# Kernel tuning notes

Measured on AMD Instinct MI355X. Metric: run time of the kernel, lower is better.

The kernel has to match this reference:

```python
import jax, jax.numpy as jnp
import numpy as np

A, M, Q, H, T = 4096, 64, 64, 64, 4
BOX_L = 20.0


def _pairwise_displacements(positions, box):
    # Minimal-image pairwise displacements. dr[i, j] = r_j - r_i (PBC-wrapped).
    diff = positions[None, :, :] - positions[:, None, :]          # [A, A, 3]
    frac = diff @ jnp.linalg.inv(box)                             # fractional coords
    frac = frac - jnp.round(frac)                                 # minimal image
    dr = frac @ box                                               # [A, A, 3]
    rij = jnp.linalg.norm(dr, axis=-1)                            # [A, A]
    return dr, rij


def _per_type_mlp(descriptors, Z, W0, b0, atom_mask):
    # a_i = q_i @ W0[Z_i] + b0[Z_i]; h = tanh(a) * mask
    W0_t = W0[Z]                                                  # [A, Q, H]
    b0_t = b0[Z]                                                  # [A, H]
    h = jnp.tanh(jnp.einsum('nd,ndh->nh', descriptors, W0_t) + b0_t)
    return h * atom_mask[:, None], W0_t


def _calc_forces(h, gradients, W1_t, W0_t, neighbor_mask):
    # dU_i/dR_j via chain rule through tanh MLP.
    dtanh = 1.0 - jnp.square(h)                                   # [A, H]
    de_da = dtanh * W1_t                                          # [A, H]
    de_dq = jnp.einsum('nh,nqh->nq', de_da, W0_t)                 # [A, Q]
    forces = jnp.einsum('nq,nmcq->nmc', de_dq, gradients)         # [A, M, 3]
    return forces * neighbor_mask[:, :, None]


def setup_inputs() -> dict:
    key = jax.random.key(0)
    ks = jax.random.split(key, 12)
    descriptors = jax.random.normal(ks[0], (A, Q), jnp.float32)
    gradients = jax.random.normal(ks[1], (A, M, 3, Q), jnp.float32)
    grad_index = jax.random.randint(ks[2], (A, M), 0, A, jnp.int32)
    positions = jax.random.uniform(ks[3], (A, 3), jnp.float32) * BOX_L
    Z = jax.random.randint(ks[4], (A,), 0, T, jnp.int32)
    box = jnp.eye(3, dtype=jnp.float32) * BOX_L
    atom_mask = jnp.ones((A,), jnp.float32)
    neighbor_mask = jnp.ones((A, M), jnp.float32)
    s = 0.05
    return {
        'descriptors': descriptors, 'gradients': gradients,
        'grad_index': grad_index, 'positions': positions, 'Z': Z,
        'box': box, 'atom_mask': atom_mask, 'neighbor_mask': neighbor_mask,
        'W0': jax.random.normal(ks[5], (T, Q, H), jnp.float32) * s,
        'b0': jnp.zeros((T, H), jnp.float32),
        'W1': jax.random.normal(ks[6], (T, H), jnp.float32) * s,
        'b1': jnp.zeros((), jnp.float32),
        'W0_pol': jax.random.normal(ks[7], (T, Q, H), jnp.float32) * s,
        'b0_pol': jnp.zeros((T, H), jnp.float32),
        'W1_pol': jax.random.normal(ks[8], (T, H), jnp.float32) * s,
        'b1_pol': jnp.zeros((), jnp.float32),
    }


def reference(descriptors, gradients, grad_index, positions, Z, box,
              atom_mask, neighbor_mask, W0, b0, W1, b1,
              W0_pol, b0_pol, W1_pol, b1_pol):
    # Tensor ANN
    h, W0_t = _per_type_mlp(descriptors, Z, W0, b0, atom_mask)
    W1_t = W1[Z]                                                  # [A, H]
    forces = _calc_forces(h, gradients, W1_t, W0_t, neighbor_mask)  # [A, M, 3]

    # Pairwise displacements + neighbor gather (tf.gather_nd equivalent)
    dr, _rij = _pairwise_displacements(positions, box)            # [A, A, 3]
    rows = jnp.arange(A)[:, None]                                 # [A, 1]
    dr_gathered = dr[rows, grad_index]                            # [A, M, 3]

    # Scalar (pol) ANN -> isotropic diagonal contribution
    h_pol, _ = _per_type_mlp(descriptors, Z, W0_pol, b0_pol, atom_mask)
    F_pol = (jnp.sum(h_pol * W1_pol[Z], axis=1) + b1_pol) * atom_mask
    scalar_sum = jnp.sum(F_pol)

    # Anisotropic virial: -sum_{n,m} dr (x) forces
    pol_outer = -jnp.einsum('nma,nmb->nmab', dr_gathered, forces)
    pol_outer = pol_outer * neighbor_mask[:, :, None, None]
    pm = jnp.sum(pol_outer, axis=(0, 1))                          # [3, 3]

    pol = jnp.stack([pm[0, 0], pm[1, 1], pm[2, 2], pm[0, 1], pm[1, 2], pm[2, 0]])
    pol = pol + jnp.stack([scalar_sum, scalar_sum, scalar_sum,
                           jnp.zeros((), pol.dtype), jnp.zeros((), pol.dtype),
                           jnp.zeros((), pol.dtype)])
    return pol
```

## Files before the change

### kernel.cpp

```cpp
#include <hip/hip_runtime.h>
#include <hip/hip_bf16.h>
#include <math.h>

#define NA 4096
#define NM 64
#define NQ 64
#define NH 64

#define WS_FLOATS (10 * NA)

__global__ __launch_bounds__(256) void tnep_fused(
    const float* __restrict__ desc,
    const float* __restrict__ grad,
    const int*   __restrict__ gidx,
    const float* __restrict__ pos,
    const int*   __restrict__ Zp,
    const float* __restrict__ box,
    const float* __restrict__ amaskp,
    const float* __restrict__ nmaskp,
    const float* __restrict__ W0,
    const float* __restrict__ b0,
    const float* __restrict__ W1,
    const float* __restrict__ W0p,
    const float* __restrict__ b0p,
    const float* __restrict__ W1p,
    const float* __restrict__ b1p,
    float* __restrict__ ws)
{
    const int n    = blockIdx.x;
    const int tid  = threadIdx.x;
    const int w    = tid >> 6;
    const int lane = tid & 63;
    const int msub = lane >> 4;
    const int q4   = lane & 15;
    const int z    = Zp[n];

    float* PARTT = ws;

    __shared__ float sW0[NQ * 65];
    __shared__ float sdesc[NQ];
    __shared__ float sde_da[NH];
    __shared__ float sde_dq[NQ];
    __shared__ float swdr[NM * 4];
    __shared__ float sacc[4][9];
    __shared__ float sfpv;

    const float4* gbase = reinterpret_cast<const float4*>(grad)
                          + ((size_t)n * NM + w * 16 + msub) * 48 + q4;
    float4 p00 = gbase[0],   p01 = gbase[16],  p02 = gbase[32];
    float4 p10 = gbase[192], p11 = gbase[208], p12 = gbase[224];

    const float4* W0v = reinterpret_cast<const float4*>(W0 + (size_t)z * NQ * NH);
#pragma unroll
    for (int i = 0; i < 4; ++i) {
        int f = i * 256 + tid;
        float4 v = W0v[f];
        int q  = f >> 4;
        int h0 = (f & 15) * 4;
        float* p = &sW0[q * 65 + h0];
        p[0] = v.x; p[1] = v.y; p[2] = v.z; p[3] = v.w;
    }
    if (w == 0) sdesc[lane] = desc[n * NQ + lane];
    if (w == 1) {
        int g = gidx[n * NM + lane];
        float Lx = box[0], Ly = box[4], Lz = box[8];
        float dx = pos[g * 3 + 0] - pos[n * 3 + 0];
        float dy = pos[g * 3 + 1] - pos[n * 3 + 1];
        float dz = pos[g * 3 + 2] - pos[n * 3 + 2];
        dx -= Lx * rintf(dx * (1.0f / Lx));
        dy -= Ly * rintf(dy * (1.0f / Ly));
        dz -= Lz * rintf(dz * (1.0f / Lz));
        float nm = nmaskp[n * NM + lane];
        float wt = -nm * nm;
        swdr[lane * 4 + 0] = wt * dx;
        swdr[lane * 4 + 1] = wt * dy;
        swdr[lane * 4 + 2] = wt * dz;
        swdr[lane * 4 + 3] = 0.0f;
    }
    __syncthreads();

    if (w == 0) {
        float amask = amaskp[n];
        float a_t = b0[z * NH + lane];
#pragma unroll 8
        for (int q = 0; q < NQ; ++q)
            a_t = fmaf(sdesc[q], sW0[q * 65 + lane], a_t);
        float hT = tanhf(a_t) * amask;
        sde_da[lane] = (1.0f - hT * hT) * W1[z * NH + lane];
        float dq = 0.0f;
#pragma unroll 8
        for (int h = 0; h < NH; ++h)
            dq = fmaf(sde_da[h], sW0[lane * 65 + h], dq);
        sde_dq[lane] = dq;
    } else if (w == 2) {
        float amask = amaskp[n];
        float a_p = b0p[z * NH + lane];
        const float* W0prow = W0p + (size_t)z * NQ * NH;
        const float* drow   = desc + (size_t)n * NQ;
#pragma unroll 8
        for (int q = 0; q < NQ; ++q)
            a_p = fmaf(drow[q], W0prow[q * NH + lane], a_p);
        float hP = tanhf(a_p) * amask;
        float fp = hP * W1p[z * NH + lane];
#pragma unroll
        for (int s = 1; s < 64; s <<= 1) fp += __shfl_xor(fp, s, 64);
        if (lane == 0) sfpv = (fp + b1p[0]) * amask;
    }
    __syncthreads();

    float4 dq4 = *reinterpret_cast<const float4*>(&sde_dq[4 * q4]);
    float acc[3][3] = {{0.f,0.f,0.f},{0.f,0.f,0.f},{0.f,0.f,0.f}};
    const int mb4 = (w * 16 + msub) * 4;

#define TNEP_DOT(g4) fmaf(dq4.x, (g4).x, fmaf(dq4.y, (g4).y, fmaf(dq4.z, (g4).z, dq4.w * (g4).w)))
#define TNEP_ACC(g0, g1, g2, widx)                                              \
    {                                                                           \
        float wd0 = swdr[(widx) + 0], wd1 = swdr[(widx) + 1], wd2 = swdr[(widx) + 2]; \
        float s0 = TNEP_DOT(g0), s1 = TNEP_DOT(g1), s2 = TNEP_DOT(g2);          \
        acc[0][0] = fmaf(s0, wd0, acc[0][0]);                                   \
        acc[1][0] = fmaf(s0, wd1, acc[1][0]);                                   \
        acc[2][0] = fmaf(s0, wd2, acc[2][0]);                                   \
        acc[0][1] = fmaf(s1, wd0, acc[0][1]);                                   \
        acc[1][1] = fmaf(s1, wd1, acc[1][1]);                                   \
        acc[2][1] = fmaf(s1, wd2, acc[2][1]);                                   \
        acc[0][2] = fmaf(s2, wd0, acc[0][2]);                                   \
        acc[1][2] = fmaf(s2, wd1, acc[1][2]);                                   \
        acc[2][2] = fmaf(s2, wd2, acc[2][2]);                                   \
    }

    TNEP_ACC(p00, p01, p02, mb4);
    TNEP_ACC(p10, p11, p12, mb4 + 16);
    {
        float4 g0 = gbase[384], g1 = gbase[400], g2 = gbase[416];
        TNEP_ACC(g0, g1, g2, mb4 + 32);
    }
    {
        float4 g0 = gbase[576], g1 = gbase[592], g2 = gbase[608];
        TNEP_ACC(g0, g1, g2, mb4 + 48);
    }
#undef TNEP_ACC
#undef TNEP_DOT

#pragma unroll
    for (int a = 0; a < 3; ++a)
#pragma unroll
        for (int c = 0; c < 3; ++c) {
            float v = acc[a][c];
#pragma unroll
            for (int s = 1; s < 64; s <<= 1) v += __shfl_xor(v, s, 64);
            if (lane == 0) sacc[w][a * 3 + c] = v;
        }
    __syncthreads();

    if (tid < 9)
        PARTT[(size_t)tid * NA + n] = sacc[0][tid] + sacc[1][tid] + sacc[2][tid] + sacc[3][tid];
    if (tid == 9)
        PARTT[(size_t)9 * NA + n] = sfpv;
}

__global__ __launch_bounds__(640) void tnep_reduce(const float* __restrict__ ws,
                                                   float* __restrict__ out)
{
    __shared__ float sred[10];
    const int w    = threadIdx.x >> 6;
    const int lane = threadIdx.x & 63;

    const float4* p = reinterpret_cast<const float4*>(ws + (size_t)w * NA);
    float s = 0.f;
#pragma unroll
    for (int i = 0; i < 16; ++i) {
        float4 v = p[lane + 64 * i];
        s += (v.x + v.y) + (v.z + v.w);
    }
#pragma unroll
    for (int t = 1; t < 64; t <<= 1) s += __shfl_xor(s, t, 64);
    if (lane == 0) sred[w] = s;
    __syncthreads();
    if (threadIdx.x == 0) {
        float S = sred[9];
        out[0] = sred[0] + S;
        out[1] = sred[4] + S;
        out[2] = sred[8] + S;
        out[3] = sred[1];
        out[4] = sred[5];
        out[5] = sred[6];
    }
}

__global__ __launch_bounds__(64) void tnep_mono(
    const float* __restrict__ desc,
    const float* __restrict__ grad,
    const int*   __restrict__ gidx,
    const float* __restrict__ pos,
    const int*   __restrict__ Zp,
    const float* __restrict__ box,
    const float* __restrict__ amaskp,
    const float* __restrict__ nmaskp,
    const float* __restrict__ W0,
    const float* __restrict__ b0,
    const float* __restrict__ W1,
    const float* __restrict__ W0p,
    const float* __restrict__ b0p,
    const float* __restrict__ W1p,
    const float* __restrict__ b1p,
    float* __restrict__ out)
{
    const int n    = blockIdx.x;
    const int lane = threadIdx.x;
    const int z    = Zp[n];
    const float amask = amaskp[n];

    __shared__ float sdesc[NQ];
    __shared__ float sW0[NQ * 65];
    __shared__ float sde_da[NH];
    __shared__ float sde_dq[NQ];
    __shared__ float sdr[NM * 4];

    sdesc[lane] = desc[n * NQ + lane];
    const float4* W0v = reinterpret_cast<const float4*>(W0 + (size_t)z * NQ * NH);
#pragma unroll
    for (int i = 0; i < 16; ++i) {
        float4 v = W0v[i * 64 + lane];
        int q  = 4 * i + (lane >> 4);
        int h0 = 4 * (lane & 15);
        float* p = &sW0[q * 65 + h0];
        p[0] = v.x; p[1] = v.y; p[2] = v.z; p[3] = v.w;
    }
    {
        int g = gidx[n * NM + lane];
        float Lx = box[0], Ly = box[4], Lz = box[8];
        float dx = pos[g * 3 + 0] - pos[n * 3 + 0];
        float dy = pos[g * 3 + 1] - pos[n * 3 + 1];
        float dz = pos[g * 3 + 2] - pos[n * 3 + 2];
        dx -= Lx * rintf(dx * (1.0f / Lx));
        dy -= Ly * rintf(dy * (1.0f / Ly));
        dz -= Lz * rintf(dz * (1.0f / Lz));
        float nm = nmaskp[n * NM + lane];
        float wt = -nm * nm;
        sdr[lane * 4 + 0] = wt * dx;
        sdr[lane * 4 + 1] = wt * dy;
        sdr[lane * 4 + 2] = wt * dz;
        sdr[lane * 4 + 3] = 0.0f;
    }
    __syncthreads();

    float a_t = b0 [z * NH + lane];
    float a_p = b0p[z * NH + lane];
    const float* W0prow = W0p + (size_t)z * NQ * NH;
#pragma unroll 8
    for (int q = 0; q < NQ; ++q) {
        float d = sdesc[q];
        a_t = fmaf(d, sW0[q * 65 + lane], a_t);
        a_p = fmaf(d, W0prow[q * NH + lane], a_p);
    }
    float hT = tanhf(a_t) * amask;
    float hP = tanhf(a_p) * amask;
    sde_da[lane] = (1.0f - hT * hT) * W1[z * NH + lane];
    float fp = hP * W1p[z * NH + lane];
#pragma unroll
    for (int s = 1; s < 64; s <<= 1) fp += __shfl_xor(fp, s, 64);
    __syncthreads();

    float dq = 0.0f;
#pragma unroll 8
    for (int h = 0; h < NH; ++h)
        dq = fmaf(sde_da[h], sW0[lane * 65 + h], dq);
    sde_dq[lane] = dq;
    __syncthreads();

    const int msub = lane >> 4;
    const int q4   = lane & 15;
    float4 dq4 = *reinterpret_cast<const float4*>(&sde_dq[4 * q4]);
    float acc[3][3] = {{0.f,0.f,0.f},{0.f,0.f,0.f},{0.f,0.f,0.f}};
    const float4* gbase = reinterpret_cast<const float4*>(grad)
                          + (size_t)n * NM * 48 + msub * 48 + q4;
#pragma unroll
    for (int gset = 0; gset < 16; ++gset) {
        const float4* gp = gbase + gset * 192;
        const int m = gset * 4 + msub;
        float wd0 = sdr[m * 4 + 0];
        float wd1 = sdr[m * 4 + 1];
        float wd2 = sdr[m * 4 + 2];
#pragma unroll
        for (int c = 0; c < 3; ++c) {
            float4 g4 = gp[c * 16];
            float s = fmaf(dq4.x, g4.x, fmaf(dq4.y, g4.y, fmaf(dq4.z, g4.z, dq4.w * g4.w)));
            acc[0][c] = fmaf(s, wd0, acc[0][c]);
            acc[1][c] = fmaf(s, wd1, acc[1][c]);
            acc[2][c] = fmaf(s, wd2, acc[2][c]);
        }
    }
    float fpv = (fp + b1p[0]) * amask;
#pragma unroll
    for (int a = 0; a < 3; ++a)
#pragma unroll
        for (int c = 0; c < 3; ++c) {
            float v = acc[a][c];
#pragma unroll
            for (int s = 1; s < 64; s <<= 1) v += __shfl_xor(v, s, 64);
            acc[a][c] = v;
        }
    if (lane == 0) {
        atomicAdd(out + 0, acc[0][0] + fpv);
        atomicAdd(out + 1, acc[1][1] + fpv);
        atomicAdd(out + 2, acc[2][2] + fpv);
        atomicAdd(out + 3, acc[0][1]);
        atomicAdd(out + 4, acc[1][2]);
        atomicAdd(out + 5, acc[2][0]);
    }
}

__global__ void tnep_zero(float* out)
{
    if (threadIdx.x < 6) out[threadIdx.x] = 0.f;
}

extern "C" void kernel_launch(void* const* d_in, const int* in_sizes, int n_in,
                              void* d_out, int out_size, void* d_ws, size_t ws_size,
                              hipStream_t stream)
{
    const float* desc  = (const float*)d_in[0];
    const float* grad  = (const float*)d_in[1];
    const int*   gidx  = (const int*)  d_in[2];
    const float* pos   = (const float*)d_in[3];
    const int*   Zp    = (const int*)  d_in[4];
    const float* box   = (const float*)d_in[5];
    const float* amask = (const float*)d_in[6];
    const float* nmask = (const float*)d_in[7];
    const float* W0    = (const float*)d_in[8];
    const float* b0    = (const float*)d_in[9];
    const float* W1    = (const float*)d_in[10];
    const float* W0p   = (const float*)d_in[12];
    const float* b0p   = (const float*)d_in[13];
    const float* W1p   = (const float*)d_in[14];
    const float* b1p   = (const float*)d_in[15];
    float* out = (float*)d_out;
    float* ws  = (float*)d_ws;

    if (ws_size >= (size_t)WS_FLOATS * sizeof(float)) {
        tnep_fused<<<NA, 256, 0, stream>>>(desc, grad, gidx, pos, Zp, box, amask, nmask,
                                           W0, b0, W1, W0p, b0p, W1p, b1p, ws);
        tnep_reduce<<<1, 640, 0, stream>>>(ws, out);
    } else {
        tnep_zero<<<1, 64, 0, stream>>>(out);
        tnep_mono<<<NA, 64, 0, stream>>>(desc, grad, gidx, pos, Zp, box, amask, nmask,
                                         W0, b0, W1, W0p, b0p, W1p, b1p, out);
    }
}
```

Measured before the change: 43.39 us.

## Process two atoms per block and split final reduction across six blocks

Result: no change. 43.65 us (+0.6%).

```diff
diff --git a/kernel.cpp b/kernel.cpp
--- a/kernel.cpp
+++ b/kernel.cpp
@@ -3,13 +3,14 @@
 #include <math.h>
 
 #define NA 4096
+#define NB (NA / 2)
 #define NM 64
 #define NQ 64
 #define NH 64
 
-#define WS_FLOATS (10 * NA)
-
-__global__ __launch_bounds__(256) void tnep_fused(
+#define WS_FLOATS (10 * NB)
+
+__global__ __launch_bounds__(256, 4) void tnep_fused2(
     const float* __restrict__ desc,
     const float* __restrict__ grad,
     const int*   __restrict__ gidx,
@@ -27,96 +28,130 @@
     const float* __restrict__ b1p,
     float* __restrict__ ws)
 {
-    const int n    = blockIdx.x;
+    const int b    = blockIdx.x;
+    const int n0   = 2 * b;
+    const int n1   = n0 + 1;
     const int tid  = threadIdx.x;
     const int w    = tid >> 6;
     const int lane = tid & 63;
     const int msub = lane >> 4;
     const int q4   = lane & 15;
-    const int z    = Zp[n];
+    const int z0   = Zp[n0];
+    const int z1   = Zp[n1];
 
     float* PARTT = ws;
 
-    __shared__ float sW0[NQ * 65];
-    __shared__ float sdesc[NQ];
-    __shared__ float sde_da[NH];
-    __shared__ float sde_dq[NQ];
-    __shared__ float swdr[NM * 4];
+    __shared__ float sW0A[NQ * 65];
+    __shared__ float sW0B[NQ * 65];
+    __shared__ float sdescA[NQ];
+    __shared__ float sdescB[NQ];
+    __shared__ float sde_da[2 * NH];
+    __shared__ float sde_dqA[NQ];
+    __shared__ float sde_dqB[NQ];
+    __shared__ float swdrA[NM * 4];
+    __shared__ float swdrB[NM * 4];
     __shared__ float sacc[4][9];
-    __shared__ float sfpv;
-
-    const float4* gbase = reinterpret_cast<const float4*>(grad)
-                          + ((size_t)n * NM + w * 16 + msub) * 48 + q4;
-    float4 p00 = gbase[0],   p01 = gbase[16],  p02 = gbase[32];
-    float4 p10 = gbase[192], p11 = gbase[208], p12 = gbase[224];
-
-    const float4* W0v = reinterpret_cast<const float4*>(W0 + (size_t)z * NQ * NH);
+    __shared__ float sfpvA, sfpvB;
+
+    const float4* gA = reinterpret_cast<const float4*>(grad)
+                       + ((size_t)n0 * NM + w * 16 + msub) * 48 + q4;
+    const float4* gB = gA + (size_t)NM * 48;
+    float4 pA0 = gA[0],   pA1 = gA[16],  pA2 = gA[32];
+    float4 pA3 = gA[192], pA4 = gA[208], pA5 = gA[224];
+    float4 pB0 = gB[0],   pB1 = gB[16],  pB2 = gB[32];
+    float4 pB3 = gB[192], pB4 = gB[208], pB5 = gB[224];
+
+    const float4* W0vA = reinterpret_cast<const float4*>(W0 + (size_t)z0 * NQ * NH);
+    const float4* W0vB = reinterpret_cast<const float4*>(W0 + (size_t)z1 * NQ * NH);
 #pragma unroll
     for (int i = 0; i < 4; ++i) {
         int f = i * 256 + tid;
-        float4 v = W0v[f];
+        float4 vA = W0vA[f];
+        float4 vB = W0vB[f];
         int q  = f >> 4;
         int h0 = (f & 15) * 4;
-        float* p = &sW0[q * 65 + h0];
-        p[0] = v.x; p[1] = v.y; p[2] = v.z; p[3] = v.w;
-    }
-    if (w == 0) sdesc[lane] = desc[n * NQ + lane];
-    if (w == 1) {
-        int g = gidx[n * NM + lane];
+        float* pa = &sW0A[q * 65 + h0];
+        pa[0] = vA.x; pa[1] = vA.y; pa[2] = vA.z; pa[3] = vA.w;
+        float* pb = &sW0B[q * 65 + h0];
+        pb[0] = vB.x; pb[1] = vB.y; pb[2] = vB.z; pb[3] = vB.w;
+    }
+    if (w == 0) sdescA[lane] = desc[n0 * NQ + lane];
+    if (w == 1) sdescB[lane] = desc[n1 * NQ + lane];
+    if (w == 2 || w == 3) {
+        const int   nn  = (w == 2) ? n0 : n1;
+        float*      sdr = (w == 2) ? swdrA : swdrB;
+        int g = gidx[nn * NM + lane];
         float Lx = box[0], Ly = box[4], Lz = box[8];
-        float dx = pos[g * 3 + 0] - pos[n * 3 + 0];
-        float dy = pos[g * 3 + 1] - pos[n * 3 + 1];
-        float dz = pos[g * 3 + 2] - pos[n * 3 + 2];
+        float dx = pos[g * 3 + 0] - pos[nn * 3 + 0];
+        float dy = pos[g * 3 + 1] - pos[nn * 3 + 1];
+        float dz = pos[g * 3 + 2] - pos[nn * 3 + 2];
         dx -= Lx * rintf(dx * (1.0f / Lx));
         dy -= Ly * rintf(dy * (1.0f / Ly));
         dz -= Lz * rintf(dz * (1.0f / Lz));
-        float nm = nmaskp[n * NM + lane];
+        float nm = nmaskp[nn * NM + lane];
         float wt = -nm * nm;
-        swdr[lane * 4 + 0] = wt * dx;
-        swdr[lane * 4 + 1] = wt * dy;
-        swdr[lane * 4 + 2] = wt * dz;
-        swdr[lane * 4 + 3] = 0.0f;
-    }
-    __syncthreads();
-
-    if (w == 0) {
-        float amask = amaskp[n];
-        float a_t = b0[z * NH + lane];
+        sdr[lane * 4 + 0] = wt * dx;
+        sdr[lane * 4 + 1] = wt * dy;
+        sdr[lane * 4 + 2] = wt * dz;
+        sdr[lane * 4 + 3] = 0.0f;
+    }
+    __syncthreads();
+
+    if (w <= 1) {
+        const int    nn   = (w == 0) ? n0 : n1;
+        const int    zz   = (w == 0) ? z0 : z1;
+        const float* sW0x = (w == 0) ? sW0A : sW0B;
+        const float* sdx  = (w == 0) ? sdescA : sdescB;
+        float*       sda  = sde_da + w * NH;
+        float*       sdq  = (w == 0) ? sde_dqA : sde_dqB;
+        float amask = amaskp[nn];
+        float a_t = b0[zz * NH + lane];
 #pragma unroll 8
         for (int q = 0; q < NQ; ++q)
-            a_t = fmaf(sdesc[q], sW0[q * 65 + lane], a_t);
+            a_t = fmaf(sdx[q], sW0x[q * 65 + lane], a_t);
         float hT = tanhf(a_t) * amask;
-        sde_da[lane] = (1.0f - hT * hT) * W1[z * NH + lane];
+        sda[lane] = (1.0f - hT * hT) * W1[zz * NH + lane];
         float dq = 0.0f;
 #pragma unroll 8
         for (int h = 0; h < NH; ++h)
-            dq = fmaf(sde_da[h], sW0[lane * 65 + h], dq);
-        sde_dq[lane] = dq;
-    } else if (w == 2) {
-        float amask = amaskp[n];
-        float a_p = b0p[z * NH + lane];
-        const float* W0prow = W0p + (size_t)z * NQ * NH;
-        const float* drow   = desc + (size_t)n * NQ;
+            dq = fmaf(sda[h], sW0x[lane * 65 + h], dq);
+        sdq[lane] = dq;
+    } else {
+        const int nn = (w == 2) ? n0 : n1;
+        const int zz = (w == 2) ? z0 : z1;
+        float amask = amaskp[nn];
+        float a_p = b0p[zz * NH + lane];
+        const float* W0prow = W0p + (size_t)zz * NQ * NH;
+        const float* drow   = desc + (size_t)nn * NQ;
 #pragma unroll 8
         for (int q = 0; q < NQ; ++q)
             a_p = fmaf(drow[q], W0prow[q * NH + lane], a_p);
         float hP = tanhf(a_p) * amask;
-        float fp = hP * W1p[z * NH + lane];
+        float fp = hP * W1p[zz * NH + lane];
 #pragma unroll
         for (int s = 1; s < 64; s <<= 1) fp += __shfl_xor(fp, s, 64);
-        if (lane == 0) sfpv = (fp + b1p[0]) * amask;
-    }
-    __syncthreads();
-
-    float4 dq4 = *reinterpret_cast<const float4*>(&sde_dq[4 * q4]);
+        if (lane == 0) {
+            float v = (fp + b1p[0]) * amask;
+            if (w == 2) sfpvA = v; else sfpvB = v;
+        }
+    }
+    __syncthreads();
+
+    float4 dq4A = *reinterpret_cast<const float4*>(&sde_dqA[4 * q4]);
+    float4 dq4B = *reinterpret_cast<const float4*>(&sde_dqB[4 * q4]);
     float acc[3][3] = {{0.f,0.f,0.f},{0.f,0.f,0.f},{0.f,0.f,0.f}};
     const int mb4 = (w * 16 + msub) * 4;
 
-#define TNEP_DOT(g4) fmaf(dq4.x, (g4).x, fmaf(dq4.y, (g4).y, fmaf(dq4.z, (g4).z, dq4.w * (g4).w)))
-#define TNEP_ACC(g0, g1, g2, widx)                                              \
+    float4 a20 = gA[384], a21 = gA[400], a22 = gA[416];
+    float4 a30 = gA[576], a31 = gA[592], a32 = gA[608];
+    float4 b20 = gB[384], b21 = gB[400], b22 = gB[416];
+    float4 b30 = gB[576], b31 = gB[592], b32 = gB[608];
+
+#define TNEP_DOT(dq4, g4) fmaf((dq4).x, (g4).x, fmaf((dq4).y, (g4).y, fmaf((dq4).z, (g4).z, (dq4).w * (g4).w)))
+#define TNEP_ACC(dq4, sdr, g0, g1, g2, widx)                                    \
     {                                                                           \
-        float wd0 = swdr[(widx) + 0], wd1 = swdr[(widx) + 1], wd2 = swdr[(widx) + 2]; \
-        float s0 = TNEP_DOT(g0), s1 = TNEP_DOT(g1), s2 = TNEP_DOT(g2);          \
+        float wd0 = (sdr)[(widx) + 0], wd1 = (sdr)[(widx) + 1], wd2 = (sdr)[(widx) + 2]; \
+        float s0 = TNEP_DOT(dq4, g0), s1 = TNEP_DOT(dq4, g1), s2 = TNEP_DOT(dq4, g2); \
         acc[0][0] = fmaf(s0, wd0, acc[0][0]);                                   \
         acc[1][0] = fmaf(s0, wd1, acc[1][0]);                                   \
         acc[2][0] = fmaf(s0, wd2, acc[2][0]);                                   \
@@ -128,16 +163,14 @@
         acc[2][2] = fmaf(s2, wd2, acc[2][2]);                                   \
     }
 
-    TNEP_ACC(p00, p01, p02, mb4);
-    TNEP_ACC(p10, p11, p12, mb4 + 16);
-    {
-        float4 g0 = gbase[384], g1 = gbase[400], g2 = gbase[416];
-        TNEP_ACC(g0, g1, g2, mb4 + 32);
-    }
-    {
-        float4 g0 = gbase[576], g1 = gbase[592], g2 = gbase[608];
-        TNEP_ACC(g0, g1, g2, mb4 + 48);
-    }
+    TNEP_ACC(dq4A, swdrA, pA0, pA1, pA2, mb4);
+    TNEP_ACC(dq4A, swdrA, pA3, pA4, pA5, mb4 + 16);
+    TNEP_ACC(dq4B, swdrB, pB0, pB1, pB2, mb4);
+    TNEP_ACC(dq4B, swdrB, pB3, pB4, pB5, mb4 + 16);
+    TNEP_ACC(dq4A, swdrA, a20, a21, a22, mb4 + 32);
+    TNEP_ACC(dq4A, swdrA, a30, a31, a32, mb4 + 48);
+    TNEP_ACC(dq4B, swdrB, b20, b21, b22, mb4 + 32);
+    TNEP_ACC(dq4B, swdrB, b30, b31, b32, mb4 + 48);
 #undef TNEP_ACC
 #undef TNEP_DOT
 
@@ -153,38 +186,38 @@
     __syncthreads();
 
     if (tid < 9)
-        PARTT[(size_t)tid * NA + n] = sacc[0][tid] + sacc[1][tid] + sacc[2][tid] + sacc[3][tid];
+        PARTT[(size_t)tid * NB + b] = sacc[0][tid] + sacc[1][tid] + sacc[2][tid] + sacc[3][tid];
     if (tid == 9)
-        PARTT[(size_t)9 * NA + n] = sfpv;
-}
-
-__global__ __launch_bounds__(640) void tnep_reduce(const float* __restrict__ ws,
-                                                   float* __restrict__ out)
-{
-    __shared__ float sred[10];
-    const int w    = threadIdx.x >> 6;
-    const int lane = threadIdx.x & 63;
-
-    const float4* p = reinterpret_cast<const float4*>(ws + (size_t)w * NA);
-    float s = 0.f;
-#pragma unroll
-    for (int i = 0; i < 16; ++i) {
-        float4 v = p[lane + 64 * i];
-        s += (v.x + v.y) + (v.z + v.w);
+        PARTT[(size_t)9 * NB + b] = sfpvA + sfpvB;
+}
+
+__global__ __launch_bounds__(256) void tnep_reduce6(const float* __restrict__ ws,
+                                                    float* __restrict__ out)
+{
+    __shared__ float sred[4];
+    const int bo   = blockIdx.x;
+    const int tid  = threadIdx.x;
+    const int w    = tid >> 6;
+    const int lane = tid & 63;
+
+    const int slotA_tab[6] = {0, 4, 8, 1, 5, 6};
+    const int slotA = slotA_tab[bo];
+    const bool hasB = (bo < 3);
+
+    const float4* pA = reinterpret_cast<const float4*>(ws + (size_t)slotA * NB);
+    const float4* pB = reinterpret_cast<const float4*>(ws + (size_t)9 * NB);
+
+    float4 v0 = pA[tid], v1 = pA[tid + 256];
+    float s = ((v0.x + v0.y) + (v0.z + v0.w)) + ((v1.x + v1.y) + (v1.z + v1.w));
+    if (hasB) {
+        float4 u0 = pB[tid], u1 = pB[tid + 256];
+        s += ((u0.x + u0.y) + (u0.z + u0.w)) + ((u1.x + u1.y) + (u1.z + u1.w));
     }
 #pragma unroll
     for (int t = 1; t < 64; t <<= 1) s += __shfl_xor(s, t, 64);
     if (lane == 0) sred[w] = s;
     __syncthreads();
-    if (threadIdx.x == 0) {
-        float S = sred[9];
-        out[0] = sred[0] + S;
-        out[1] = sred[4] + S;
-        out[2] = sred[8] + S;
-        out[3] = sred[1];
-        out[4] = sred[5];
-        out[5] = sred[6];
-    }
+    if (tid == 0) out[bo] = (sred[0] + sred[1]) + (sred[2] + sred[3]);
 }
 
 __global__ __launch_bounds__(64) void tnep_mono(
@@ -338,9 +371,9 @@
     float* ws  = (float*)d_ws;
 
     if (ws_size >= (size_t)WS_FLOATS * sizeof(float)) {
-        tnep_fused<<<NA, 256, 0, stream>>>(desc, grad, gidx, pos, Zp, box, amask, nmask,
-                                           W0, b0, W1, W0p, b0p, W1p, b1p, ws);
-        tnep_reduce<<<1, 640, 0, stream>>>(ws, out);
+        tnep_fused2<<<NB, 256, 0, stream>>>(desc, grad, gidx, pos, Zp, box, amask, nmask,
+                                            W0, b0, W1, W0p, b0p, W1p, b1p, ws);
+        tnep_reduce6<<<6, 256, 0, stream>>>(ws, out);
     } else {
         tnep_zero<<<1, 64, 0, stream>>>(out);
         tnep_mono<<<NA, 64, 0, stream>>>(desc, grad, gidx, pos, Zp, box, amask, nmask,
```
